# Performance work log

Measured on AMD Instinct MI355X. Metric: run time of the kernel, lower is better.

## Reference

```python
import jax, jax.numpy as jnp
import numpy as np

EMBED = 768; DEPTH = 4; BATCH = 4; SEQ = 1024
DIN = 2 * EMBED          # expand=2
DSTATE = 16; DCONV = 4; DTRANK = 48  # ceil(768/16)
EPS = 1e-5


def setup_inputs() -> dict:
    key = jax.random.key(0)
    ks = jax.random.split(key, 10)
    s = 0.02
    A_log = jnp.tile(jnp.log(jnp.arange(1, DSTATE + 1, dtype=jnp.float32)), (DEPTH, DIN, 1))
    return {
        "x_mamba": jax.random.normal(ks[0], (BATCH, SEQ, EMBED), jnp.float32),
        "x_attn": jax.random.normal(ks[1], (BATCH, SEQ, EMBED), jnp.float32),
        "W_in": jax.random.normal(ks[2], (DEPTH, 2 * DIN, EMBED), jnp.float32) * s,
        "W_extra": jax.random.normal(ks[3], (DEPTH, DIN, EMBED), jnp.float32) * s,
        "conv_w": jax.random.normal(ks[4], (DEPTH, DIN, DCONV), jnp.float32) * s,
        "conv_b": jnp.zeros((DEPTH, DIN), jnp.float32),
        "W_xproj": jax.random.normal(ks[5], (DEPTH, DTRANK + 2 * DSTATE, DIN), jnp.float32) * s,
        "W_dt": jax.random.normal(ks[6], (DEPTH, DIN, DTRANK), jnp.float32) * s,
        "b_dt": jnp.full((DEPTH, DIN), -4.6, jnp.float32),  # softplus -> dt ~ 0.01
        "A_log": A_log,
        "D_skip": jnp.ones((DEPTH, DIN), jnp.float32),
        "W_out": jax.random.normal(ks[7], (DEPTH, EMBED, DIN), jnp.float32) * s,
        "norm_w": jnp.ones((DEPTH, EMBED), jnp.float32),
        "normf_w": jnp.ones((EMBED,), jnp.float32),
        "normf_b": jnp.zeros((EMBED,), jnp.float32),
    }


def rmsnorm(x, w, b=None, eps=EPS):
    x = x.astype(jnp.float32)
    y = x * jax.lax.rsqrt(jnp.mean(x * x, axis=-1, keepdims=True) + eps) * w
    return y if b is None else y + b


def causal_conv1d(x, w, b):
    # depthwise causal conv: x (B,L,D), w (D,K)
    K = w.shape[-1]; L = x.shape[1]
    xp = jnp.pad(x, ((0, 0), (K - 1, 0), (0, 0)))
    y = b
    for k in range(K):
        y = y + xp[:, k:k + L] * w[:, k]
    return y


def selective_scan(u, dt, A, Bm, Cm):
    # u, dt: (B,L,D); A: (D,N); Bm, Cm: (B,L,N)
    def step(h, inp):
        u_t, dt_t, B_t, C_t = inp  # (B,D),(B,D),(B,N),(B,N)
        h = jnp.exp(dt_t[..., None] * A) * h + (dt_t * u_t)[..., None] * B_t[:, None, :]
        return h, jnp.einsum('bdn,bn->bd', h, C_t)
    h0 = jnp.zeros((u.shape[0], u.shape[2], A.shape[1]), u.dtype)
    xs = (jnp.swapaxes(u, 0, 1), jnp.swapaxes(dt, 0, 1),
          jnp.swapaxes(Bm, 0, 1), jnp.swapaxes(Cm, 0, 1))
    _, ys = jax.lax.scan(step, h0, xs)
    return jnp.swapaxes(ys, 0, 1)  # (B,L,D)


def cross_mamba_mixer(h, extra, W_in, W_extra, conv_w, conv_b, W_xproj, W_dt, b_dt, A_log, D_skip, W_out):
    xz = jnp.einsum('ble,fe->blf', h, W_in)        # (B,L,2*DIN)
    x, z = jnp.split(xz, 2, axis=-1)
    u = jax.nn.silu(causal_conv1d(x, conv_w, conv_b))  # SSM input from x_mamba stream
    e = jax.nn.silu(jnp.einsum('ble,de->bld', extra, W_extra))  # selection params from cross stream
    dbl = jnp.einsum('bld,rd->blr', e, W_xproj)
    dt_low = dbl[..., :DTRANK]
    Bm = dbl[..., DTRANK:DTRANK + DSTATE]
    Cm = dbl[..., DTRANK + DSTATE:]
    dt = jax.nn.softplus(jnp.einsum('blr,dr->bld', dt_low, W_dt) + b_dt)
    A = -jnp.exp(A_log)
    y = selective_scan(u, dt, A, Bm, Cm) + u * D_skip
    return jnp.einsum('bld,ed->ble', y * jax.nn.silu(z), W_out)


def reference(x_mamba, x_attn, W_in, W_extra, conv_w, conv_b, W_xproj, W_dt, b_dt, A_log, D_skip, W_out, norm_w, normf_w, normf_b):
    hidden = x_mamba
    residual = None
    for i in range(DEPTH):
        # fused add + RMSNorm (prenorm), residual kept in fp32; drop_path = identity at eval
        residual = hidden.astype(jnp.float32) if residual is None else residual + hidden.astype(jnp.float32)
        hn = rmsnorm(residual, norm_w[i]).astype(x_mamba.dtype)
        hidden = cross_mamba_mixer(hn, x_attn, W_in[i], W_extra[i], conv_w[i], conv_b[i],
                                   W_xproj[i], W_dt[i], b_dt[i], A_log[i], D_skip[i], W_out[i])
    out = rmsnorm(hidden.astype(jnp.float32) + residual, normf_w, normf_b)
    return out.astype(x_mamba.dtype)
```

## Files before the change

kernel.cpp:

```cpp
#include <hip/hip_runtime.h>

#define EMBED  768
#define DEPTH  4
#define BATCH  4
#define SEQL   1024
#define DIN    1536
#define NSTATE 16
#define DCONV  4
#define DTRANK 48
#define MROWS  (BATCH*SEQL)
#define NCHUNK 64
#define CLEN   (SEQL/NCHUNK)

typedef __attribute__((ext_vector_type(8))) short s16x8;
typedef __attribute__((ext_vector_type(4))) float f32x4;

__device__ __forceinline__ float fsilu(float x) { return x / (1.0f + __expf(-x)); }
__device__ __forceinline__ float fsoftplus(float x) {
    return (x > 20.f) ? x : __logf(1.0f + __expf(x));
}

__device__ __forceinline__ unsigned short f2bf(float f) {
    union { float f; unsigned u; } v; v.f = f;
    unsigned r = v.u + 0x7fffu + ((v.u >> 16) & 1u);
    return (unsigned short)(r >> 16);
}
__device__ __forceinline__ float bf2f(unsigned short s) {
    union { unsigned u; float f; } v; v.u = ((unsigned)s) << 16; return v.f;
}
__device__ __forceinline__ float bflo(unsigned w) {
    union { unsigned u; float f; } v; v.u = w << 16; return v.f;
}
__device__ __forceinline__ float bfhi(unsigned w) {
    union { unsigned u; float f; } v; v.u = w & 0xffff0000u; return v.f;
}

typedef const __attribute__((address_space(1))) void gvoid_t;
typedef __attribute__((address_space(3))) void lvoid_t;
__device__ __forceinline__ void gload16(const void* g, void* l) {
    __builtin_amdgcn_global_load_lds((gvoid_t*)g, (lvoid_t*)l, 16, 0, 0);
}

__device__ __forceinline__ void powers16(float e1, float* ep) {
    float e2 = e1 * e1, e3 = e1 * e2, e4 = e2 * e2;
    float e5 = e2 * e3, e6 = e3 * e3, e7 = e3 * e4, e8 = e4 * e4;
    ep[0] = e1;      ep[1] = e2;      ep[2] = e3;      ep[3] = e4;
    ep[4] = e5;      ep[5] = e6;      ep[6] = e7;      ep[7] = e8;
    ep[8] = e4 * e5; ep[9] = e5 * e5; ep[10] = e5 * e6; ep[11] = e6 * e6;
    ep[12] = e6 * e7; ep[13] = e7 * e7; ep[14] = e7 * e8; ep[15] = e8 * e8;
}

#define N_WIN  ((long long)DEPTH*2*DIN*EMBED)
#define N_WEX  ((long long)DEPTH*DIN*EMBED)
#define N_WXP  ((long long)DEPTH*128*DIN)
#define N_WOUT ((long long)DEPTH*EMBED*DIN)
#define N_XAT  ((long long)MROWS*EMBED)
#define N_WDT  ((long long)DEPTH*DIN*64)
#define N_ALL  (N_WIN + N_WEX + N_WXP + N_WOUT + N_XAT + N_WDT)

__global__ __launch_bounds__(256)
void cvt_all_kernel(const float* __restrict__ w_in, const float* __restrict__ w_ex,
                    const float* __restrict__ w_xp, const float* __restrict__ w_out,
                    const float* __restrict__ x_at, const float* __restrict__ w_dt,
                    unsigned short* __restrict__ o_in, unsigned short* __restrict__ o_ex,
                    unsigned short* __restrict__ o_xp, unsigned short* __restrict__ o_out,
                    unsigned short* __restrict__ o_at, unsigned short* __restrict__ o_dt)
{
    long long i = (long long)blockIdx.x * 256 + threadIdx.x;
    long long stride = (long long)gridDim.x * 256;
    for (; i < N_ALL; i += stride) {
        long long j = i;
        if (j < N_WIN)  { o_in[j]  = f2bf(w_in[j]);  continue; }
        j -= N_WIN;
        if (j < N_WEX)  { o_ex[j]  = f2bf(w_ex[j]);  continue; }
        j -= N_WEX;
        if (j < N_WXP)  {
            long long l = j / (128 * DIN);
            int r = (int)((j / DIN) & 127);
            int k = (int)(j % DIN);
            o_xp[j] = (r < 80) ? f2bf(w_xp[(l * 80 + r) * DIN + k]) : (unsigned short)0;
            continue;
        }
        j -= N_WXP;
        if (j < N_WOUT) { o_out[j] = f2bf(w_out[j]); continue; }
        j -= N_WOUT;
        if (j < N_XAT)  { o_at[j]  = f2bf(x_at[j]);  continue; }
        j -= N_XAT;
        { int rd = (int)(j >> 6), n = (int)(j & 63);
          o_dt[j] = (n < DTRANK) ? f2bf(w_dt[rd * DTRANK + n]) : (unsigned short)0; }
    }
}

template<int EPI>
__global__ __launch_bounds__(256)
void gemm128_kernel(const unsigned short* __restrict__ A0,
                    const unsigned short* __restrict__ W0,
                    unsigned short* __restrict__ outB0,
                    unsigned short* __restrict__ outB2,
                    const float* __restrict__ bias0,
                    int N, int K, int ldC, int gridx,
                    long long sAz, long long sWz, long long sOz, long long sBz)
{
    __shared__ unsigned short smem[2 * 3 * 128 * 32];
    unsigned short* lA = smem;
    unsigned short* lB = smem + 3 * 128 * 32;

    const unsigned short* A = A0 + (size_t)blockIdx.z * sAz;
    const unsigned short* W = W0 + (size_t)blockIdx.z * sWz;
    unsigned short* outB = outB0 + (size_t)blockIdx.z * sOz;
    const float* bias = bias0 + (size_t)blockIdx.z * sBz;

    const int nwg = gridx * 32;
    const int cpx = nwg >> 3;
    int bid = blockIdx.x;
    int lid = (bid & 7) * cpx + (bid >> 3);
    const int GM  = 8;
    int grp = lid / (GM * gridx);
    int rem = lid - grp * (GM * gridx);
    const int by = grp * GM + (rem % GM);
    const int bx = rem / GM;
    const int m0 = by * 128;
    const int n0 = bx * 128;

    const int tid  = threadIdx.x;
    const int lane = tid & 63;
    const int w    = tid >> 6;
    const int wm   = w >> 1, wn = w & 1;

    const int rloc = lane >> 2;
    const int cg   = (lane & 3) ^ ((lane >> 3) & 3);
    const unsigned short* gA = A + (size_t)(m0 + w * 32 + rloc) * K + cg * 8;
    const unsigned short* gB = W + (size_t)(n0 + w * 32 + rloc) * K + cg * 8;

    const int fr   = lane & 15;
    const int g    = lane >> 4;
    const int slot = g ^ ((fr >> 1) & 3);
    const int aRd  = (wm * 64 + fr) * 32 + slot * 8;
    const int bRd  = (wn * 64 + fr) * 32 + slot * 8;

    f32x4 acc[4][4];
    #pragma unroll
    for (int i = 0; i < 4; ++i)
        #pragma unroll
        for (int j = 0; j < 4; ++j) acc[i][j] = f32x4{0.f, 0.f, 0.f, 0.f};

    auto stage = [&](int buf, int k0) {
        unsigned short* la = lA + buf * 4096 + w * 1024;
        unsigned short* lb = lB + buf * 4096 + w * 1024;
        gload16(gA + k0,          la);
        gload16(gA + k0 + 16 * K, la + 512);
        gload16(gB + k0,          lb);
        gload16(gB + k0 + 16 * K, lb + 512);
    };

    const int NT = K >> 5;
    stage(0, 0);
    if (NT > 1) stage(1, 32);

    for (int t = 0; t < NT; ++t) {
        if (t + 1 < NT) asm volatile("s_waitcnt vmcnt(4)" ::: "memory");
        else            asm volatile("s_waitcnt vmcnt(0)" ::: "memory");
        __builtin_amdgcn_s_barrier();
        if (t + 2 < NT) stage((t + 2) % 3, (t + 2) * 32);

        const int cur = (t % 3) * 4096;
        s16x8 af[4], bfr[4];
        #pragma unroll
        for (int i = 0; i < 4; ++i) af[i]  = *(const s16x8*)&lA[cur + aRd + i * 512];
        #pragma unroll
        for (int j = 0; j < 4; ++j) bfr[j] = *(const s16x8*)&lB[cur + bRd + j * 512];
        #pragma unroll
        for (int i = 0; i < 4; ++i)
            #pragma unroll
            for (int j = 0; j < 4; ++j)
                asm("v_mfma_f32_16x16x32_bf16 %0, %1, %2, %0"
                    : "+v"(acc[i][j]) : "v"(af[i]), "v"(bfr[j]));
    }
    asm volatile("s_nop 7\n\ts_nop 7"
                 : "+v"(acc[0][0]), "+v"(acc[0][1]), "+v"(acc[0][2]), "+v"(acc[0][3]),
                   "+v"(acc[1][0]), "+v"(acc[1][1]), "+v"(acc[1][2]), "+v"(acc[1][3]));
    asm volatile("s_nop 7\n\ts_nop 7"
                 : "+v"(acc[2][0]), "+v"(acc[2][1]), "+v"(acc[2][2]), "+v"(acc[2][3]),
                   "+v"(acc[3][0]), "+v"(acc[3][1]), "+v"(acc[3][2]), "+v"(acc[3][3]));

    __syncthreads();
    unsigned short* ot = smem;
    #pragma unroll
    for (int i = 0; i < 4; ++i) {
        #pragma unroll
        for (int j = 0; j < 4; ++j) {
            int col = wn * 64 + j * 16 + fr;
            #pragma unroll
            for (int r = 0; r < 4; ++r) {
                int row = wm * 64 + i * 16 + g * 4 + r;
                float vv = acc[i][j][r];
                unsigned short o;
                if (EPI == 2)      o = f2bf(fsoftplus(vv + bias[n0 + col]));
                else if (EPI == 1 || EPI == 4) o = f2bf(fsilu(vv));
                else               o = f2bf(vv);
                ot[row * 132 + col] = o;
            }
        }
    }
    __syncthreads();
    unsigned short* dst;
    int ld;
    if (EPI == 3) {
        dst = (n0 < DIN) ? (outB + n0) : (outB2 + (n0 - DIN));
        ld = DIN;
    } else if (EPI == 4) {
        int l = n0 / DIN;
        dst = outB + (size_t)l * MROWS * DIN + (n0 - l * DIN);
        ld = DIN;
    } else {
        dst = outB + n0;
        ld = ldC;
    }
    const int rw = tid >> 4;
    const int cc = (tid & 15) * 8;
    #pragma unroll
    for (int it = 0; it < 8; ++it) {
        int row = it * 16 + rw;
        s16x8 v = *(const s16x8*)&ot[row * 132 + cc];
        *(s16x8*)&dst[(size_t)(m0 + row) * ld + cc] = v;
    }
}

__global__ __launch_bounds__(256)
void gemm_xproj_kernel(const unsigned short* __restrict__ Aall,
                       const unsigned short* __restrict__ Wall,
                       float* __restrict__ dblAll,
                       unsigned short* __restrict__ dtlAll)
{
    __shared__ unsigned short lA[3 * 128 * 32];
    __shared__ unsigned short lB[3 * 128 * 32];
    const int l = blockIdx.z;
    const int K = DIN;
    const unsigned short* A = Aall + (size_t)l * MROWS * DIN;
    const unsigned short* W = Wall + (size_t)l * 128 * DIN;
    float* outF = dblAll + (size_t)l * MROWS * 80;
    unsigned short* outB = dtlAll + (size_t)l * MROWS * 64;

    int bid = blockIdx.x;
    int lid = (bid & 7) * 4 + (bid >> 3);
    const int m0 = lid * 128;
    const int n0 = 0;

    const int tid  = threadIdx.x;
    const int lane = tid & 63;
    const int w    = tid >> 6;
    const int wm   = w >> 1, wn = w & 1;

    const int rloc = lane >> 2;
    const int cg   = (lane & 3) ^ ((lane >> 3) & 3);
    const unsigned short* gA = A + (size_t)(m0 + w * 32 + rloc) * K + cg * 8;
    const unsigned short* gB = W + (size_t)(n0 + w * 32 + rloc) * K + cg * 8;

    const int fr   = lane & 15;
    const int g    = lane >> 4;
    const int slot = g ^ ((fr >> 1) & 3);
    const int aRd  = (wm * 64 + fr) * 32 + slot * 8;
    const int bRd  = (wn * 64 + fr) * 32 + slot * 8;

    f32x4 acc[4][4];
    #pragma unroll
    for (int i = 0; i < 4; ++i)
        #pragma unroll
        for (int j = 0; j < 4; ++j) acc[i][j] = f32x4{0.f, 0.f, 0.f, 0.f};

    auto stage = [&](int buf, int k0) {
        unsigned short* la = lA + buf * 4096 + w * 1024;
        unsigned short* lb = lB + buf * 4096 + w * 1024;
        gload16(gA + k0,          la);
        gload16(gA + k0 + 16 * K, la + 512);
        gload16(gB + k0,          lb);
        gload16(gB + k0 + 16 * K, lb + 512);
    };

    const int NT = K >> 5;
    stage(0, 0);
    stage(1, 32);

    for (int t = 0; t < NT; ++t) {
        if (t + 1 < NT) asm volatile("s_waitcnt vmcnt(4)" ::: "memory");
        else            asm volatile("s_waitcnt vmcnt(0)" ::: "memory");
        __builtin_amdgcn_s_barrier();
        if (t + 2 < NT) stage((t + 2) % 3, (t + 2) * 32);

        const int cur = (t % 3) * 4096;
        s16x8 af[4], bfr[4];
        #pragma unroll
        for (int i = 0; i < 4; ++i) af[i]  = *(const s16x8*)&lA[cur + aRd + i * 512];
        #pragma unroll
        for (int j = 0; j < 4; ++j) bfr[j] = *(const s16x8*)&lB[cur + bRd + j * 512];
        #pragma unroll
        for (int i = 0; i < 4; ++i)
            #pragma unroll
            for (int j = 0; j < 4; ++j)
                asm("v_mfma_f32_16x16x32_bf16 %0, %1, %2, %0"
                    : "+v"(acc[i][j]) : "v"(af[i]), "v"(bfr[j]));
    }
    asm volatile("s_nop 7\n\ts_nop 7"
                 : "+v"(acc[0][0]), "+v"(acc[0][1]), "+v"(acc[0][2]), "+v"(acc[0][3]),
                   "+v"(acc[1][0]), "+v"(acc[1][1]), "+v"(acc[1][2]), "+v"(acc[1][3]));
    asm volatile("s_nop 7\n\ts_nop 7"
                 : "+v"(acc[2][0]), "+v"(acc[2][1]), "+v"(acc[2][2]), "+v"(acc[2][3]),
                   "+v"(acc[3][0]), "+v"(acc[3][1]), "+v"(acc[3][2]), "+v"(acc[3][3]));

    #pragma unroll
    for (int i = 0; i < 4; ++i) {
        #pragma unroll
        for (int j = 0; j < 4; ++j) {
            int col = wn * 64 + j * 16 + fr;
            #pragma unroll
            for (int r = 0; r < 4; ++r) {
                int row = m0 + wm * 64 + i * 16 + g * 4 + r;
                float vv = acc[i][j][r];
                if (col < 80)      outF[(size_t)row * 80 + col] = vv;
                if (col < DTRANK)  outB[(size_t)row * 64 + col] = f2bf(vv);
                else if (col < 64) outB[(size_t)row * 64 + col] = 0;
            }
        }
    }
}

__global__ __launch_bounds__(256)
void gemm_wout_kernel(const unsigned short* __restrict__ A,
                      const unsigned short* __restrict__ W,
                      float* __restrict__ outF,
                      int N, int K, int ldC, int gridx)
{
    __shared__ unsigned short lA[3 * 128 * 32];
    __shared__ unsigned short lB[3 * 64 * 32];

    const int nwg = gridx * 32;
    const int cpx = nwg >> 3;
    int bid = blockIdx.x;
    int lid = (bid & 7) * cpx + (bid >> 3);
    const int GM  = 8;
    int grp = lid / (GM * gridx);
    int rem = lid - grp * (GM * gridx);
    const int by = grp * GM + (rem % GM);
    const int bx = rem / GM;
    const int m0 = by * 128;
    const int n0 = bx * 64;

    const int tid  = threadIdx.x;
    const int lane = tid & 63;
    const int w    = tid >> 6;

    const int rloc = lane >> 2;
    const int cg   = (lane & 3) ^ ((lane >> 3) & 3);
    const unsigned short* gA = A + (size_t)(m0 + w * 32 + rloc) * K + cg * 8;
    const unsigned short* gB = W + (size_t)(n0 + w * 16 + rloc) * K + cg * 8;

    const int fr   = lane & 15;
    const int g    = lane >> 4;
    const int slot = g ^ ((fr >> 1) & 3);
    const int aRd  = (w * 32 + fr) * 32 + slot * 8;
    const int bRd  = fr * 32 + slot * 8;

    f32x4 acc[2][4];
    #pragma unroll
    for (int i = 0; i < 2; ++i)
        #pragma unroll
        for (int j = 0; j < 4; ++j) acc[i][j] = f32x4{0.f, 0.f, 0.f, 0.f};

    auto stage = [&](int buf, int k0) {
        unsigned short* la = lA + buf * 4096 + w * 1024;
        unsigned short* lb = lB + buf * 2048 + w * 512;
        gload16(gA + k0,          la);
        gload16(gA + k0 + 16 * K, la + 512);
        gload16(gB + k0,          lb);
    };

    const int NT = K >> 5;
    stage(0, 0);
    stage(1, 32);

    for (int t = 0; t < NT; ++t) {
        if (t + 1 < NT) asm volatile("s_waitcnt vmcnt(3)" ::: "memory");
        else            asm volatile("s_waitcnt vmcnt(0)" ::: "memory");
        __builtin_amdgcn_s_barrier();
        if (t + 2 < NT) stage((t + 2) % 3, (t + 2) * 32);

        const int cA = (t % 3) * 4096;
        const int cB = (t % 3) * 2048;
        s16x8 af[2], bfr[4];
        #pragma unroll
        for (int i = 0; i < 2; ++i) af[i]  = *(const s16x8*)&lA[cA + aRd + i * 512];
        #pragma unroll
        for (int j = 0; j < 4; ++j) bfr[j] = *(const s16x8*)&lB[cB + bRd + j * 512];
        #pragma unroll
        for (int i = 0; i < 2; ++i)
            #pragma unroll
            for (int j = 0; j < 4; ++j)
                asm("v_mfma_f32_16x16x32_bf16 %0, %1, %2, %0"
                    : "+v"(acc[i][j]) : "v"(af[i]), "v"(bfr[j]));
    }
    asm volatile("s_nop 7\n\ts_nop 7"
                 : "+v"(acc[0][0]), "+v"(acc[0][1]), "+v"(acc[0][2]), "+v"(acc[0][3]),
                   "+v"(acc[1][0]), "+v"(acc[1][1]), "+v"(acc[1][2]), "+v"(acc[1][3]));

    #pragma unroll
    for (int i = 0; i < 2; ++i) {
        #pragma unroll
        for (int j = 0; j < 4; ++j) {
            int col = n0 + j * 16 + fr;
            #pragma unroll
            for (int r = 0; r < 4; ++r) {
                int row = m0 + w * 32 + i * 16 + g * 4 + r;
                outF[(size_t)row * ldC + col] = acc[i][j][r];
            }
        }
    }
}

__global__ __launch_bounds__(256)
void rmsnorm_layer_kernel(const float* __restrict__ hid,
                          float* __restrict__ resid,
                          const float* __restrict__ w,
                          unsigned short* __restrict__ hnB,
                          int add)
{
    __shared__ float sred[4];
    int row = blockIdx.x, tid = threadIdx.x;
    size_t base = (size_t)row * EMBED;
    float x0 = hid[base + tid];
    float x1 = hid[base + tid + 256];
    float x2 = hid[base + tid + 512];
    if (add) { x0 += resid[base + tid]; x1 += resid[base + tid + 256]; x2 += resid[base + tid + 512]; }
    float ss = x0 * x0 + x1 * x1 + x2 * x2;
    #pragma unroll
    for (int o = 1; o < 64; o <<= 1) ss += __shfl_xor(ss, o);
    if ((tid & 63) == 0) sred[tid >> 6] = ss;
    __syncthreads();
    float rstd = rsqrtf((sred[0] + sred[1] + sred[2] + sred[3]) * (1.0f / EMBED) + 1e-5f);
    resid[base + tid]       = x0;
    resid[base + tid + 256] = x1;
    resid[base + tid + 512] = x2;
    hnB[base + tid]       = f2bf(x0 * rstd * w[tid]);
    hnB[base + tid + 256] = f2bf(x1 * rstd * w[tid + 256]);
    hnB[base + tid + 512] = f2bf(x2 * rstd * w[tid + 512]);
}

__global__ __launch_bounds__(256)
void final_norm_kernel(const float* __restrict__ hid,
                       const float* __restrict__ resid,
                       const float* __restrict__ wf,
                       const float* __restrict__ bfv,
                       float* __restrict__ out)
{
    __shared__ float sred[4];
    int row = blockIdx.x, tid = threadIdx.x;
    size_t base = (size_t)row * EMBED;
    float x0 = hid[base + tid]       + resid[base + tid];
    float x1 = hid[base + tid + 256] + resid[base + tid + 256];
    float x2 = hid[base + tid + 512] + resid[base + tid + 512];
    float ss = x0 * x0 + x1 * x1 + x2 * x2;
    #pragma unroll
    for (int o = 1; o < 64; o <<= 1) ss += __shfl_xor(ss, o);
    if ((tid & 63) == 0) sred[tid >> 6] = ss;
    __syncthreads();
    float rstd = rsqrtf((sred[0] + sred[1] + sred[2] + sred[3]) * (1.0f / EMBED) + 1e-5f);
    out[base + tid]       = x0 * rstd * wf[tid]       + bfv[tid];
    out[base + tid + 256] = x1 * rstd * wf[tid + 256] + bfv[tid + 256];
    out[base + tid + 512] = x2 * rstd * wf[tid + 512] + bfv[tid + 512];
}


__global__ __launch_bounds__(256)
void scan1_kernel(const unsigned short* __restrict__ xB,
                  const unsigned short* __restrict__ dt,
                  const float* __restrict__ dbl,
                  const float* __restrict__ cw, const float* __restrict__ cb,
                  float* __restrict__ SH, float* __restrict__ Cs)
{
    int tid = threadIdx.x;
    int d0 = blockIdx.y * 512 + tid * 2;
    int chunk = blockIdx.x, b = blockIdx.z;
    __shared__ float sB[CLEN][NSTATE];
    size_t row0 = (size_t)b * SEQL + (size_t)chunk * CLEN;
    { int t = tid >> 4, n = tid & 15;
      sB[t][n] = dbl[(row0 + t) * 80 + DTRANK + n]; }
    __syncthreads();

    f32x4 cw0 = *(const f32x4*)&cw[d0 * 4];
    f32x4 cw1 = *(const f32x4*)&cw[d0 * 4 + 4];
    float cb0 = cb[d0], cb1 = cb[d0 + 1];
    float xa3 = 0.f, xa2 = 0.f, xa1 = 0.f, xb3 = 0.f, xb2 = 0.f, xb1 = 0.f;
    if (chunk > 0) {
        unsigned m3 = *(const unsigned*)&xB[(row0 - 3) * DIN + d0];
        unsigned m2 = *(const unsigned*)&xB[(row0 - 2) * DIN + d0];
        unsigned m1 = *(const unsigned*)&xB[(row0 - 1) * DIN + d0];
        xa3 = bflo(m3); xb3 = bfhi(m3);
        xa2 = bflo(m2); xb2 = bfhi(m2);
        xa1 = bflo(m1); xb1 = bfhi(m1);
    }

    f32x4 S0[4], S1[4];
    #pragma unroll
    for (int i = 0; i < 4; ++i) { S0[i] = f32x4{0.f,0.f,0.f,0.f}; S1[i] = S0[i]; }
    float cs0 = 0.f, cs1 = 0.f;
    const unsigned* dtp = (const unsigned*)(dt + row0 * DIN + d0);
    const unsigned* xp  = (const unsigned*)(xB + row0 * DIN + d0);
    for (int t = 0; t < CLEN; ++t) {
        unsigned xw = *xp, dw = *dtp;
        float xc0 = bflo(xw), xc1 = bfhi(xw);
        float uv0 = fsilu(cb0 + cw0[0]*xa3 + cw0[1]*xa2 + cw0[2]*xa1 + cw0[3]*xc0);
        float uv1 = fsilu(cb1 + cw1[0]*xb3 + cw1[1]*xb2 + cw1[2]*xb1 + cw1[3]*xc1);
        xa3 = xa2; xa2 = xa1; xa1 = xc0;
        xb3 = xb2; xb2 = xb1; xb1 = xc1;
        float dt0 = bflo(dw), dt1 = bfhi(dw);
        cs0 += dt0; cs1 += dt1;
        float du0 = dt0 * uv0, du1 = dt1 * uv1;
        float ep0[16], ep1[16];
        powers16(__expf(-dt0), ep0);
        powers16(__expf(-dt1), ep1);
        #pragma unroll
        for (int i = 0; i < 4; ++i) {
            f32x4 Bv = *(const f32x4*)&sB[t][4 * i];
            #pragma unroll
            for (int k = 0; k < 4; ++k) {
                S0[i][k] = fmaf(ep0[i * 4 + k], S0[i][k], du0 * Bv[k]);
                S1[i][k] = fmaf(ep1[i * 4 + k], S1[i][k], du1 * Bv[k]);
            }
        }
        dtp += DIN / 2; xp += DIN / 2;
    }
    size_t o16 = (((size_t)chunk * BATCH + b) * DIN + d0) * 16;
    #pragma unroll
    for (int i = 0; i < 4; ++i) *(f32x4*)&SH[o16 + 4 * i]      = S0[i];
    #pragma unroll
    for (int i = 0; i < 4; ++i) *(f32x4*)&SH[o16 + 16 + 4 * i] = S1[i];
    size_t ci = ((size_t)chunk * BATCH + b) * DIN + d0;
    Cs[ci] = cs0; Cs[ci + 1] = cs1;
}

__global__ __launch_bounds__(256)
void scan2_kernel(float* __restrict__ SH, const float* __restrict__ Cs)
{
    int j = blockIdx.x * 256 + threadIdx.x;
    int n  = j & 15;
    int bd = j >> 4;
    float nf = (float)(n + 1);
    const int stride16 = BATCH * DIN * 16;
    const int stride1  = BATCH * DIN;
    float h = 0.f;
    #pragma unroll 4
    for (int c = 0; c < NCHUNK; ++c) {
        size_t o = (size_t)c * stride16 + j;
        float s = SH[o];
        SH[o] = h;
        float P = __expf(-Cs[(size_t)c * stride1 + bd] * nf);
        h = s + P * h;
    }
}

__global__ __launch_bounds__(256)
void scan3_kernel(const unsigned short* __restrict__ xB,
                  const unsigned short* __restrict__ dt,
                  const float* __restrict__ dbl,
                  const unsigned short* __restrict__ z,
                  const float* __restrict__ cw, const float* __restrict__ cb,
                  const float* __restrict__ Dskip,
                  const float* __restrict__ SH, unsigned short* __restrict__ g)
{
    int tid = threadIdx.x;
    int d0 = blockIdx.y * 512 + tid * 2;
    int chunk = blockIdx.x, b = blockIdx.z;
    __shared__ float sB[CLEN][NSTATE];
    __shared__ float sC[CLEN][NSTATE];
    size_t row0 = (size_t)b * SEQL + (size_t)chunk * CLEN;
    { int t = tid >> 4, n = tid & 15;
      sB[t][n] = dbl[(row0 + t) * 80 + DTRANK + n];
      sC[t][n] = dbl[(row0 + t) * 80 + DTRANK + NSTATE + n]; }
    __syncthreads();

    f32x4 cw0 = *(const f32x4*)&cw[d0 * 4];
    f32x4 cw1 = *(const f32x4*)&cw[d0 * 4 + 4];
    float cb0 = cb[d0], cb1 = cb[d0 + 1];
    float Ds0 = Dskip[d0], Ds1 = Dskip[d0 + 1];
    float xa3 = 0.f, xa2 = 0.f, xa1 = 0.f, xb3 = 0.f, xb2 = 0.f, xb1 = 0.f;
    if (chunk > 0) {
        unsigned m3 = *(const unsigned*)&xB[(row0 - 3) * DIN + d0];
        unsigned m2 = *(const unsigned*)&xB[(row0 - 2) * DIN + d0];
        unsigned m1 = *(const unsigned*)&xB[(row0 - 1) * DIN + d0];
        xa3 = bflo(m3); xb3 = bfhi(m3);
        xa2 = bflo(m2); xb2 = bfhi(m2);
        xa1 = bflo(m1); xb1 = bfhi(m1);
    }

    size_t o16 = (((size_t)chunk * BATCH + b) * DIN + d0) * 16;
    f32x4 h0[4], h1[4];
    #pragma unroll
    for (int i = 0; i < 4; ++i) h0[i] = *(const f32x4*)&SH[o16 + 4 * i];
    #pragma unroll
    for (int i = 0; i < 4; ++i) h1[i] = *(const f32x4*)&SH[o16 + 16 + 4 * i];

    const unsigned* dtp = (const unsigned*)(dt + row0 * DIN + d0);
    const unsigned* xp  = (const unsigned*)(xB + row0 * DIN + d0);
    const unsigned* zp  = (const unsigned*)(z  + row0 * DIN + d0);
    unsigned* gp = (unsigned*)(g + row0 * DIN + d0);
    for (int t = 0; t < CLEN; ++t) {
        unsigned xw = *xp, dw = *dtp, zw = *zp;
        float xc0 = bflo(xw), xc1 = bfhi(xw);
        float uv0 = fsilu(cb0 + cw0[0]*xa3 + cw0[1]*xa2 + cw0[2]*xa1 + cw0[3]*xc0);
        float uv1 = fsilu(cb1 + cw1[0]*xb3 + cw1[1]*xb2 + cw1[2]*xb1 + cw1[3]*xc1);
        xa3 = xa2; xa2 = xa1; xa1 = xc0;
        xb3 = xb2; xb2 = xb1; xb1 = xc1;
        float dt0 = bflo(dw), dt1 = bfhi(dw);
        float du0 = dt0 * uv0, du1 = dt1 * uv1;
        float ep0[16], ep1[16];
        powers16(__expf(-dt0), ep0);
        powers16(__expf(-dt1), ep1);
        float p0 = 0.f, p1 = 0.f;
        #pragma unroll
        for (int i = 0; i < 4; ++i) {
            f32x4 Bv = *(const f32x4*)&sB[t][4 * i];
            f32x4 Cv = *(const f32x4*)&sC[t][4 * i];
            #pragma unroll
            for (int k = 0; k < 4; ++k) {
                h0[i][k] = fmaf(ep0[i * 4 + k], h0[i][k], du0 * Bv[k]);
                h1[i][k] = fmaf(ep1[i * 4 + k], h1[i][k], du1 * Bv[k]);
                p0 = fmaf(h0[i][k], Cv[k], p0);
                p1 = fmaf(h1[i][k], Cv[k], p1);
            }
        }
        float g0 = (p0 + uv0 * Ds0) * fsilu(bflo(zw));
        float g1 = (p1 + uv1 * Ds1) * fsilu(bfhi(zw));
        *gp = (unsigned)f2bf(g0) | ((unsigned)f2bf(g1) << 16);
        dtp += DIN / 2; xp += DIN / 2; zp += DIN / 2; gp += DIN / 2;
    }
}

extern "C" void kernel_launch(void* const* d_in, const int* in_sizes, int n_in,
                              void* d_out, int out_size, void* d_ws, size_t ws_size,
                              hipStream_t stream)
{
    (void)in_sizes; (void)n_in; (void)out_size; (void)ws_size;
    const float* x_mamba = (const float*)d_in[0];
    const float* x_attn  = (const float*)d_in[1];
    const float* W_in    = (const float*)d_in[2];
    const float* W_extra = (const float*)d_in[3];
    const float* conv_w  = (const float*)d_in[4];
    const float* conv_b  = (const float*)d_in[5];
    const float* W_xproj = (const float*)d_in[6];
    const float* W_dt    = (const float*)d_in[7];
    const float* b_dt    = (const float*)d_in[8];
    const float* D_skip  = (const float*)d_in[10];
    const float* W_out   = (const float*)d_in[11];
    const float* norm_w  = (const float*)d_in[12];
    const float* normf_w = (const float*)d_in[13];
    const float* normf_b = (const float*)d_in[14];
    float* out = (float*)d_out;

    char* ws = (char*)d_ws;
    size_t off = 0;
    auto alloc = [&](size_t bytes) -> char* {
        char* p = ws + off;
        off = (off + bytes + 255) & ~(size_t)255;
        return p;
    };

    unsigned short* wInB   = (unsigned short*)alloc((size_t)DEPTH * 2 * DIN * EMBED * 2);
    unsigned short* wExB   = (unsigned short*)alloc((size_t)DEPTH * DIN * EMBED * 2);
    unsigned short* wXpB   = (unsigned short*)alloc((size_t)DEPTH * 128 * DIN * 2);
    unsigned short* wDtB   = (unsigned short*)alloc((size_t)DEPTH * DIN * 64 * 2);
    unsigned short* wOutB  = (unsigned short*)alloc((size_t)DEPTH * EMBED * DIN * 2);
    unsigned short* xattnB = (unsigned short*)alloc((size_t)MROWS * EMBED * 2);
    unsigned short* hnB    = (unsigned short*)alloc((size_t)MROWS * EMBED * 2);
    unsigned short* eAll   = (unsigned short*)alloc((size_t)DEPTH * MROWS * DIN * 2);
    unsigned short* dtlAll = (unsigned short*)alloc((size_t)DEPTH * MROWS * 64 * 2);
    float*          dblAll = (float*)alloc((size_t)DEPTH * MROWS * 80 * 4);
    unsigned short* dtAll  = (unsigned short*)alloc((size_t)DEPTH * MROWS * DIN * 2);
    unsigned short* gB     = (unsigned short*)alloc((size_t)MROWS * DIN * 2);
    unsigned short* zB     = (unsigned short*)alloc((size_t)MROWS * DIN * 2);
    unsigned short* xB     = (unsigned short*)alloc((size_t)MROWS * DIN * 2);
    float* resid  = (float*)alloc((size_t)MROWS * EMBED * 4);
    float* hidden = (float*)alloc((size_t)MROWS * EMBED * 4);
    float* SH     = (float*)alloc((size_t)NCHUNK * BATCH * DIN * 16 * 4);
    float* Cs     = (float*)alloc((size_t)NCHUNK * BATCH * DIN * 4);

    cvt_all_kernel<<<4096, 256, 0, stream>>>(W_in, W_extra, W_xproj, W_out, x_attn, W_dt,
                                             wInB, wExB, wXpB, wOutB, xattnB, wDtB);

    gemm128_kernel<4><<<48 * 32, 256, 0, stream>>>(
        xattnB, wExB, eAll, nullptr, nullptr, 4 * DIN, EMBED, 4 * DIN, 48, 0, 0, 0, 0);
    gemm_xproj_kernel<<<dim3(32, 1, DEPTH), 256, 0, stream>>>(eAll, wXpB, dblAll, dtlAll);
    gemm128_kernel<2><<<dim3(12 * 32, 1, DEPTH), 256, 0, stream>>>(
        dtlAll, wDtB, dtAll, nullptr, b_dt, DIN, 64, DIN, 12,
        (long long)MROWS * 64, (long long)DIN * 64, (long long)MROWS * DIN, DIN);

    for (int l = 0; l < DEPTH; ++l) {
        rmsnorm_layer_kernel<<<MROWS, 256, 0, stream>>>(
            l == 0 ? x_mamba : (const float*)hidden, resid, norm_w + l * EMBED, hnB, l > 0 ? 1 : 0);

        gemm128_kernel<3><<<24 * 32, 256, 0, stream>>>(
            hnB, wInB + (size_t)l * 2 * DIN * EMBED, xB, zB, nullptr,
            2 * DIN, EMBED, DIN, 24, 0, 0, 0, 0);

        const float* dbl_l = dblAll + (size_t)l * MROWS * 80;
        const unsigned short* dt_l = dtAll + (size_t)l * MROWS * DIN;
        scan1_kernel<<<dim3(NCHUNK, DIN / 512, BATCH), 256, 0, stream>>>(
            xB, dt_l, dbl_l, conv_w + l * DIN * DCONV, conv_b + l * DIN, SH, Cs);
        scan2_kernel<<<(BATCH * DIN * 16) / 256, 256, 0, stream>>>(SH, Cs);
        scan3_kernel<<<dim3(NCHUNK, DIN / 512, BATCH), 256, 0, stream>>>(
            xB, dt_l, dbl_l, zB, conv_w + l * DIN * DCONV, conv_b + l * DIN,
            D_skip + l * DIN, SH, gB);

        gemm_wout_kernel<<<12 * 32, 256, 0, stream>>>(
            gB, wOutB + (size_t)l * EMBED * DIN, hidden, EMBED, DIN, EMBED, 12);
    }

    final_norm_kernel<<<MROWS, 256, 0, stream>>>(hidden, resid, normf_w, normf_b, out);
}
```

Before: 696.7 us.

## Fuse three chunked-scan kernels into one cooperative kernel with grid syncs

Merges the chunk-local scan, the cross-chunk prefix pass, and the output scan into one cooperative kernel separated by grid-wide barriers. This removes two kernel launches and their inter-kernel gaps per layer and keeps the sB/sC shared tiles loaded across phases. The grid is 768 blocks of 256 threads, which must all be co-resident for the cooperative launch to work. The middle phase uses only 384 of those blocks, and grid.sync adds its own barrier cost. A dead EPI==1 epilogue branch is also removed.

```diff
diff --git a/kernel.cpp b/kernel.cpp
--- a/kernel.cpp
+++ b/kernel.cpp
@@ -1,4 +1,6 @@
 #include <hip/hip_runtime.h>
+#include <hip/hip_cooperative_groups.h>
+namespace cg = cooperative_groups;
 
 #define EMBED  768
 #define DEPTH  4
@@ -196,7 +198,7 @@
                 float vv = acc[i][j][r];
                 unsigned short o;
                 if (EPI == 2)      o = f2bf(fsoftplus(vv + bias[n0 + col]));
-                else if (EPI == 1 || EPI == 4) o = f2bf(fsilu(vv));
+                else if (EPI == 4) o = f2bf(fsilu(vv));
                 else               o = f2bf(vv);
                 ot[row * 132 + col] = o;
             }
@@ -468,104 +470,17 @@
     out[base + tid + 512] = x2 * rstd * wf[tid + 512] + bfv[tid + 512];
 }
 
-
 __global__ __launch_bounds__(256)
-void scan1_kernel(const unsigned short* __restrict__ xB,
-                  const unsigned short* __restrict__ dt,
-                  const float* __restrict__ dbl,
-                  const float* __restrict__ cw, const float* __restrict__ cb,
-                  float* __restrict__ SH, float* __restrict__ Cs)
+void scan_fused_kernel(const unsigned short* __restrict__ xB,
+                       const unsigned short* __restrict__ dt,
+                       const float* __restrict__ dbl,
+                       const unsigned short* __restrict__ z,
+                       const float* __restrict__ cw, const float* __restrict__ cb,
+                       const float* __restrict__ Dskip,
+                       float* __restrict__ SH, float* __restrict__ Cs,
+                       unsigned short* __restrict__ g)
 {
-    int tid = threadIdx.x;
-    int d0 = blockIdx.y * 512 + tid * 2;
-    int chunk = blockIdx.x, b = blockIdx.z;
-    __shared__ float sB[CLEN][NSTATE];
-    size_t row0 = (size_t)b * SEQL + (size_t)chunk * CLEN;
-    { int t = tid >> 4, n = tid & 15;
-      sB[t][n] = dbl[(row0 + t) * 80 + DTRANK + n]; }
-    __syncthreads();
-
-    f32x4 cw0 = *(const f32x4*)&cw[d0 * 4];
-    f32x4 cw1 = *(const f32x4*)&cw[d0 * 4 + 4];
-    float cb0 = cb[d0], cb1 = cb[d0 + 1];
-    float xa3 = 0.f, xa2 = 0.f, xa1 = 0.f, xb3 = 0.f, xb2 = 0.f, xb1 = 0.f;
-    if (chunk > 0) {
-        unsigned m3 = *(const unsigned*)&xB[(row0 - 3) * DIN + d0];
-        unsigned m2 = *(const unsigned*)&xB[(row0 - 2) * DIN + d0];
-        unsigned m1 = *(const unsigned*)&xB[(row0 - 1) * DIN + d0];
-        xa3 = bflo(m3); xb3 = bfhi(m3);
-        xa2 = bflo(m2); xb2 = bfhi(m2);
-        xa1 = bflo(m1); xb1 = bfhi(m1);
-    }
-
-    f32x4 S0[4], S1[4];
-    #pragma unroll
-    for (int i = 0; i < 4; ++i) { S0[i] = f32x4{0.f,0.f,0.f,0.f}; S1[i] = S0[i]; }
-    float cs0 = 0.f, cs1 = 0.f;
-    const unsigned* dtp = (const unsigned*)(dt + row0 * DIN + d0);
-    const unsigned* xp  = (const unsigned*)(xB + row0 * DIN + d0);
-    for (int t = 0; t < CLEN; ++t) {
-        unsigned xw = *xp, dw = *dtp;
-        float xc0 = bflo(xw), xc1 = bfhi(xw);
-        float uv0 = fsilu(cb0 + cw0[0]*xa3 + cw0[1]*xa2 + cw0[2]*xa1 + cw0[3]*xc0);
-        float uv1 = fsilu(cb1 + cw1[0]*xb3 + cw1[1]*xb2 + cw1[2]*xb1 + cw1[3]*xc1);
-        xa3 = xa2; xa2 = xa1; xa1 = xc0;
-        xb3 = xb2; xb2 = xb1; xb1 = xc1;
-        float dt0 = bflo(dw), dt1 = bfhi(dw);
-        cs0 += dt0; cs1 += dt1;
-        float du0 = dt0 * uv0, du1 = dt1 * uv1;
-        float ep0[16], ep1[16];
-        powers16(__expf(-dt0), ep0);
-        powers16(__expf(-dt1), ep1);
-        #pragma unroll
-        for (int i = 0; i < 4; ++i) {
-            f32x4 Bv = *(const f32x4*)&sB[t][4 * i];
-            #pragma unroll
-            for (int k = 0; k < 4; ++k) {
-                S0[i][k] = fmaf(ep0[i * 4 + k], S0[i][k], du0 * Bv[k]);
-                S1[i][k] = fmaf(ep1[i * 4 + k], S1[i][k], du1 * Bv[k]);
-            }
-        }
-        dtp += DIN / 2; xp += DIN / 2;
-    }
-    size_t o16 = (((size_t)chunk * BATCH + b) * DIN + d0) * 16;
-    #pragma unroll
-    for (int i = 0; i < 4; ++i) *(f32x4*)&SH[o16 + 4 * i]      = S0[i];
-    #pragma unroll
-    for (int i = 0; i < 4; ++i) *(f32x4*)&SH[o16 + 16 + 4 * i] = S1[i];
-    size_t ci = ((size_t)chunk * BATCH + b) * DIN + d0;
-    Cs[ci] = cs0; Cs[ci + 1] = cs1;
-}
-
-__global__ __launch_bounds__(256)
-void scan2_kernel(float* __restrict__ SH, const float* __restrict__ Cs)
-{
-    int j = blockIdx.x * 256 + threadIdx.x;
-    int n  = j & 15;
-    int bd = j >> 4;
-    float nf = (float)(n + 1);
-    const int stride16 = BATCH * DIN * 16;
-    const int stride1  = BATCH * DIN;
-    float h = 0.f;
-    #pragma unroll 4
-    for (int c = 0; c < NCHUNK; ++c) {
-        size_t o = (size_t)c * stride16 + j;
-        float s = SH[o];
-        SH[o] = h;
-        float P = __expf(-Cs[(size_t)c * stride1 + bd] * nf);
-        h = s + P * h;
-    }
-}
-
-__global__ __launch_bounds__(256)
-void scan3_kernel(const unsigned short* __restrict__ xB,
-                  const unsigned short* __restrict__ dt,
-                  const float* __restrict__ dbl,
-                  const unsigned short* __restrict__ z,
-                  const float* __restrict__ cw, const float* __restrict__ cb,
-                  const float* __restrict__ Dskip,
-                  const float* __restrict__ SH, unsigned short* __restrict__ g)
-{
+    cg::grid_group grid = cg::this_grid();
     int tid = threadIdx.x;
     int d0 = blockIdx.y * 512 + tid * 2;
     int chunk = blockIdx.x, b = blockIdx.z;
@@ -580,57 +495,126 @@
     f32x4 cw0 = *(const f32x4*)&cw[d0 * 4];
     f32x4 cw1 = *(const f32x4*)&cw[d0 * 4 + 4];
     float cb0 = cb[d0], cb1 = cb[d0 + 1];
-    float Ds0 = Dskip[d0], Ds1 = Dskip[d0 + 1];
-    float xa3 = 0.f, xa2 = 0.f, xa1 = 0.f, xb3 = 0.f, xb2 = 0.f, xb1 = 0.f;
+    float ia3 = 0.f, ia2 = 0.f, ia1 = 0.f, ib3 = 0.f, ib2 = 0.f, ib1 = 0.f;
     if (chunk > 0) {
         unsigned m3 = *(const unsigned*)&xB[(row0 - 3) * DIN + d0];
         unsigned m2 = *(const unsigned*)&xB[(row0 - 2) * DIN + d0];
         unsigned m1 = *(const unsigned*)&xB[(row0 - 1) * DIN + d0];
-        xa3 = bflo(m3); xb3 = bfhi(m3);
-        xa2 = bflo(m2); xb2 = bfhi(m2);
-        xa1 = bflo(m1); xb1 = bfhi(m1);
-    }
-
+        ia3 = bflo(m3); ib3 = bfhi(m3);
+        ia2 = bflo(m2); ib2 = bfhi(m2);
+        ia1 = bflo(m1); ib1 = bfhi(m1);
+    }
     size_t o16 = (((size_t)chunk * BATCH + b) * DIN + d0) * 16;
-    f32x4 h0[4], h1[4];
-    #pragma unroll
-    for (int i = 0; i < 4; ++i) h0[i] = *(const f32x4*)&SH[o16 + 4 * i];
-    #pragma unroll
-    for (int i = 0; i < 4; ++i) h1[i] = *(const f32x4*)&SH[o16 + 16 + 4 * i];
-
-    const unsigned* dtp = (const unsigned*)(dt + row0 * DIN + d0);
-    const unsigned* xp  = (const unsigned*)(xB + row0 * DIN + d0);
-    const unsigned* zp  = (const unsigned*)(z  + row0 * DIN + d0);
-    unsigned* gp = (unsigned*)(g + row0 * DIN + d0);
-    for (int t = 0; t < CLEN; ++t) {
-        unsigned xw = *xp, dw = *dtp, zw = *zp;
-        float xc0 = bflo(xw), xc1 = bfhi(xw);
-        float uv0 = fsilu(cb0 + cw0[0]*xa3 + cw0[1]*xa2 + cw0[2]*xa1 + cw0[3]*xc0);
-        float uv1 = fsilu(cb1 + cw1[0]*xb3 + cw1[1]*xb2 + cw1[2]*xb1 + cw1[3]*xc1);
-        xa3 = xa2; xa2 = xa1; xa1 = xc0;
-        xb3 = xb2; xb2 = xb1; xb1 = xc1;
-        float dt0 = bflo(dw), dt1 = bfhi(dw);
-        float du0 = dt0 * uv0, du1 = dt1 * uv1;
-        float ep0[16], ep1[16];
-        powers16(__expf(-dt0), ep0);
-        powers16(__expf(-dt1), ep1);
-        float p0 = 0.f, p1 = 0.f;
-        #pragma unroll
-        for (int i = 0; i < 4; ++i) {
-            f32x4 Bv = *(const f32x4*)&sB[t][4 * i];
-            f32x4 Cv = *(const f32x4*)&sC[t][4 * i];
+    const unsigned* dtp0 = (const unsigned*)(dt + row0 * DIN + d0);
+    const unsigned* xp0  = (const unsigned*)(xB + row0 * DIN + d0);
+
+    {
+        float xa3 = ia3, xa2 = ia2, xa1 = ia1, xb3 = ib3, xb2 = ib2, xb1 = ib1;
+        f32x4 S0[4], S1[4];
+        #pragma unroll
+        for (int i = 0; i < 4; ++i) { S0[i] = f32x4{0.f,0.f,0.f,0.f}; S1[i] = S0[i]; }
+        float cs0 = 0.f, cs1 = 0.f;
+        const unsigned* dtp = dtp0;
+        const unsigned* xp  = xp0;
+        for (int t = 0; t < CLEN; ++t) {
+            unsigned xw = *xp, dw = *dtp;
+            float xc0 = bflo(xw), xc1 = bfhi(xw);
+            float uv0 = fsilu(cb0 + cw0[0]*xa3 + cw0[1]*xa2 + cw0[2]*xa1 + cw0[3]*xc0);
+            float uv1 = fsilu(cb1 + cw1[0]*xb3 + cw1[1]*xb2 + cw1[2]*xb1 + cw1[3]*xc1);
+            xa3 = xa2; xa2 = xa1; xa1 = xc0;
+            xb3 = xb2; xb2 = xb1; xb1 = xc1;
+            float dt0 = bflo(dw), dt1 = bfhi(dw);
+            cs0 += dt0; cs1 += dt1;
+            float du0 = dt0 * uv0, du1 = dt1 * uv1;
+            float ep0[16], ep1[16];
+            powers16(__expf(-dt0), ep0);
+            powers16(__expf(-dt1), ep1);
             #pragma unroll
-            for (int k = 0; k < 4; ++k) {
-                h0[i][k] = fmaf(ep0[i * 4 + k], h0[i][k], du0 * Bv[k]);
-                h1[i][k] = fmaf(ep1[i * 4 + k], h1[i][k], du1 * Bv[k]);
-                p0 = fmaf(h0[i][k], Cv[k], p0);
-                p1 = fmaf(h1[i][k], Cv[k], p1);
+            for (int i = 0; i < 4; ++i) {
+                f32x4 Bv = *(const f32x4*)&sB[t][4 * i];
+                #pragma unroll
+                for (int k = 0; k < 4; ++k) {
+                    S0[i][k] = fmaf(ep0[i * 4 + k], S0[i][k], du0 * Bv[k]);
+                    S1[i][k] = fmaf(ep1[i * 4 + k], S1[i][k], du1 * Bv[k]);
+                }
+            }
+            dtp += DIN / 2; xp += DIN / 2;
+        }
+        #pragma unroll
+        for (int i = 0; i < 4; ++i) *(f32x4*)&SH[o16 + 4 * i]      = S0[i];
+        #pragma unroll
+        for (int i = 0; i < 4; ++i) *(f32x4*)&SH[o16 + 16 + 4 * i] = S1[i];
+        size_t ci = ((size_t)chunk * BATCH + b) * DIN + d0;
+        Cs[ci] = cs0; Cs[ci + 1] = cs1;
+    }
+
+    grid.sync();
+
+    {
+        int fb = blockIdx.x + NCHUNK * (blockIdx.y + (DIN / 512) * blockIdx.z);
+        if (fb < (BATCH * DIN * 16) / 256) {
+            int j = fb * 256 + tid;
+            int n  = j & 15;
+            int bd = j >> 4;
+            float nf = (float)(n + 1);
+            const int stride16 = BATCH * DIN * 16;
+            const int stride1  = BATCH * DIN;
+            float h = 0.f;
+            #pragma unroll 4
+            for (int c = 0; c < NCHUNK; ++c) {
+                size_t o = (size_t)c * stride16 + j;
+                float s = SH[o];
+                SH[o] = h;
+                float P = __expf(-Cs[(size_t)c * stride1 + bd] * nf);
+                h = s + P * h;
             }
         }
-        float g0 = (p0 + uv0 * Ds0) * fsilu(bflo(zw));
-        float g1 = (p1 + uv1 * Ds1) * fsilu(bfhi(zw));
-        *gp = (unsigned)f2bf(g0) | ((unsigned)f2bf(g1) << 16);
-        dtp += DIN / 2; xp += DIN / 2; zp += DIN / 2; gp += DIN / 2;
+    }
+
+    grid.sync();
+
+    {
+        float xa3 = ia3, xa2 = ia2, xa1 = ia1, xb3 = ib3, xb2 = ib2, xb1 = ib1;
+        float Ds0 = Dskip[d0], Ds1 = Dskip[d0 + 1];
+        f32x4 h0[4], h1[4];
+        #pragma unroll
+        for (int i = 0; i < 4; ++i) h0[i] = *(const f32x4*)&SH[o16 + 4 * i];
+        #pragma unroll
+        for (int i = 0; i < 4; ++i) h1[i] = *(const f32x4*)&SH[o16 + 16 + 4 * i];
+        const unsigned* dtp = dtp0;
+        const unsigned* xp  = xp0;
+        const unsigned* zp  = (const unsigned*)(z + row0 * DIN + d0);
+        unsigned* gp = (unsigned*)(g + row0 * DIN + d0);
+        for (int t = 0; t < CLEN; ++t) {
+            unsigned xw = *xp, dw = *dtp, zw = *zp;
+            float xc0 = bflo(xw), xc1 = bfhi(xw);
+            float uv0 = fsilu(cb0 + cw0[0]*xa3 + cw0[1]*xa2 + cw0[2]*xa1 + cw0[3]*xc0);
+            float uv1 = fsilu(cb1 + cw1[0]*xb3 + cw1[1]*xb2 + cw1[2]*xb1 + cw1[3]*xc1);
+            xa3 = xa2; xa2 = xa1; xa1 = xc0;
+            xb3 = xb2; xb2 = xb1; xb1 = xc1;
+            float dt0 = bflo(dw), dt1 = bfhi(dw);
+            float du0 = dt0 * uv0, du1 = dt1 * uv1;
+            float ep0[16], ep1[16];
+            powers16(__expf(-dt0), ep0);
+            powers16(__expf(-dt1), ep1);
+            float p0 = 0.f, p1 = 0.f;
+            #pragma unroll
+            for (int i = 0; i < 4; ++i) {
+                f32x4 Bv = *(const f32x4*)&sB[t][4 * i];
+                f32x4 Cv = *(const f32x4*)&sC[t][4 * i];
+                #pragma unroll
+                for (int k = 0; k < 4; ++k) {
+                    h0[i][k] = fmaf(ep0[i * 4 + k], h0[i][k], du0 * Bv[k]);
+                    h1[i][k] = fmaf(ep1[i * 4 + k], h1[i][k], du1 * Bv[k]);
+                    p0 = fmaf(h0[i][k], Cv[k], p0);
+                    p1 = fmaf(h1[i][k], Cv[k], p1);
+                }
+            }
+            float g0 = (p0 + uv0 * Ds0) * fsilu(bflo(zw));
+            float g1 = (p1 + uv1 * Ds1) * fsilu(bfhi(zw));
+            *gp = (unsigned)f2bf(g0) | ((unsigned)f2bf(g1) << 16);
+            dtp += DIN / 2; xp += DIN / 2; zp += DIN / 2; gp += DIN / 2;
+        }
     }
 }
 
@@ -700,14 +684,22 @@
             hnB, wInB + (size_t)l * 2 * DIN * EMBED, xB, zB, nullptr,
             2 * DIN, EMBED, DIN, 24, 0, 0, 0, 0);
 
-        const float* dbl_l = dblAll + (size_t)l * MROWS * 80;
-        const unsigned short* dt_l = dtAll + (size_t)l * MROWS * DIN;
-        scan1_kernel<<<dim3(NCHUNK, DIN / 512, BATCH), 256, 0, stream>>>(
-            xB, dt_l, dbl_l, conv_w + l * DIN * DCONV, conv_b + l * DIN, SH, Cs);
-        scan2_kernel<<<(BATCH * DIN * 16) / 256, 256, 0, stream>>>(SH, Cs);
-        scan3_kernel<<<dim3(NCHUNK, DIN / 512, BATCH), 256, 0, stream>>>(
-            xB, dt_l, dbl_l, zB, conv_w + l * DIN * DCONV, conv_b + l * DIN,
-            D_skip + l * DIN, SH, gB);
+        {
+            const unsigned short* xBc = xB;
+            const unsigned short* dtc = dtAll + (size_t)l * MROWS * DIN;
+            const float* dblc = dblAll + (size_t)l * MROWS * 80;
+            const unsigned short* zc = zB;
+            const float* cwc = conv_w + l * DIN * DCONV;
+            const float* cbc = conv_b + l * DIN;
+            const float* dsc = D_skip + l * DIN;
+            float* SHc = SH; float* Csc = Cs;
+            unsigned short* gc = gB;
+            void* args[] = { (void*)&xBc, (void*)&dtc, (void*)&dblc, (void*)&zc,
+                             (void*)&cwc, (void*)&cbc, (void*)&dsc,
+                             (void*)&SHc, (void*)&Csc, (void*)&gc };
+            hipLaunchCooperativeKernel((void*)scan_fused_kernel,
+                dim3(NCHUNK, DIN / 512, BATCH), dim3(256), args, 0, stream);
+        }
 
         gemm_wout_kernel<<<12 * 32, 256, 0, stream>>>(
             gB, wOutB + (size_t)l * EMBED * DIN, hidden, EMBED, DIN, EMBED, 12);
```

Result: slower. 1.464 ms (+110.2%).
